# Kernel tuning notes

Measured on AMD Instinct MI355X. Metric: run time of the kernel, lower is better.

## Reference

```python
import jax, jax.numpy as jnp
import numpy as np

ALPHA = 8.3  # depth-similarity decay from Depth-aware CNN
K = 3        # kernel size
PAD = 1      # padding (stride=1, dilation=1)


def _patches(x, k, pad):
    """Extract kxk stride-1 patches. x: (B,C,H,W) -> (B,C,k,k,H,W)."""
    B, C, H, W = x.shape
    xp = jnp.pad(x, ((0, 0), (0, 0), (pad, pad), (pad, pad)))
    rows = []
    for i in range(k):
        cols = [xp[:, :, i:i + H, j:j + W] for j in range(k)]
        rows.append(jnp.stack(cols, axis=2))          # (B,C,k,H,W)
    return jnp.stack(rows, axis=2)                     # (B,C,k,k,H,W)


def setup_inputs() -> dict:
    key = jax.random.key(0)
    k1, k2, k3 = jax.random.split(key, 3)
    B, Cin, H, W = 8, 512, 64, 64
    Cout = 64
    x = jax.random.normal(k1, (B, Cin, H, W), dtype=jnp.float32)
    depth = jax.random.uniform(k2, (B, 1, H, W), dtype=jnp.float32)
    stdv = 1.0 / np.sqrt(Cin * K * K)
    weight = jax.random.uniform(k3, (Cout, Cin, K, K), dtype=jnp.float32,
                                minval=-stdv, maxval=stdv)
    return {"input": x, "depth": depth, "weight": weight}


def reference(input, depth, weight):
    # depth-modulated conv: out(p0) = sum_pn w(pn) * x(p0+pn) * exp(-a*|d(p0)-d(p0+pn)|)
    xpat = _patches(input, K, PAD)                 # (B,Cin,K,K,H,W)
    dpat = _patches(depth, K, PAD)                 # (B,1,K,K,H,W)
    d0 = depth[:, :, None, None, :, :]             # center depth (B,1,1,1,H,W)
    gate = jnp.exp(-ALPHA * jnp.abs(d0 - dpat))    # (B,1,K,K,H,W)
    out = jnp.einsum('ocij,bcijhw->bohw', weight, xpat * gate)
    return out
```

## Files before the change

### kernel.cpp

```cpp
#include <hip/hip_runtime.h>
#include <math.h>

#define ALPHA 8.3f
#define STAGE_BYTES 26112

typedef short v8s  __attribute__((ext_vector_type(8)));
typedef float v16f __attribute__((ext_vector_type(16)));
typedef float v4f  __attribute__((ext_vector_type(4)));

static __device__ __forceinline__ unsigned short f2bf(float f) {
    unsigned int u = __float_as_uint(f);
    u = (u + 0x7fffu + ((u >> 16) & 1u)) >> 16;
    return (unsigned short)u;
}

static __device__ __forceinline__ void async16(const void* g, void* l) {
    __builtin_amdgcn_global_load_lds(
        (const __attribute__((address_space(1))) unsigned int*)g,
        (__attribute__((address_space(3))) unsigned int*)l, 16, 0, 0);
}

__global__ void prep_weights(const float* __restrict__ w, unsigned short* __restrict__ wt) {
    int i = blockIdx.x * 256 + threadIdx.x;
    if (i >= 9 * 32 * 2 * 64 * 8) return;
    int j    = i & 7;
    int lane = (i >> 3) & 63;
    int mt   = (i >> 9) & 1;
    int ks   = (i >> 10) & 31;
    int tap  = i >> 15;
    int o = mt * 32 + (lane & 31);
    int c = ks * 16 + (lane >> 5) * 8 + j;
    wt[i] = f2bf(w[(o * 512 + c) * 9 + tap]);
}

__global__ __launch_bounds__(256) void nhwc_cast(const float* __restrict__ x,
                                                 unsigned short* __restrict__ x2) {
    __shared__ float st[64][65];
    const int h = blockIdx.x & 63;
    const int b = blockIdx.x >> 6;
    const int tid = threadIdx.x;
    const float* xb = x + ((size_t)b * 512) * 4096 + h * 64;
    unsigned short* ob = x2 + (((size_t)b * 64 + h) * 64) * 512;
    for (int cb = 0; cb < 8; ++cb) {
        __syncthreads();
#pragma unroll
        for (int i = 0; i < 16; ++i) {
            const int c = i * 4 + (tid >> 6);
            st[c][tid & 63] = xb[(size_t)(cb * 64 + c) * 4096 + (tid & 63)];
        }
        __syncthreads();
#pragma unroll
        for (int j = 0; j < 2; ++j) {
            const int idx = j * 256 + tid;
            const int w = idx >> 3, k = idx & 7;
            unsigned short t[8];
#pragma unroll
            for (int e = 0; e < 8; ++e) t[e] = f2bf(st[k * 8 + e][w]);
            uint4 u;
            u.x = t[0] | ((unsigned)t[1] << 16);
            u.y = t[2] | ((unsigned)t[3] << 16);
            u.z = t[4] | ((unsigned)t[5] << 16);
            u.w = t[6] | ((unsigned)t[7] << 16);
            *(uint4*)&ob[(size_t)w * 512 + cb * 64 + k * 8] = u;
        }
    }
}

__global__ __launch_bounds__(512, 2)
void depthconv_v5(const unsigned short* __restrict__ x2,
                  const float* __restrict__ depth,
                  const unsigned short* __restrict__ wt,
                  const float* __restrict__ zbuf,
                  float* __restrict__ out) {
    __shared__ __align__(16) char smem[2 * STAGE_BYTES];

    const int bx   = blockIdx.x;
    const int xcd  = bx & 7;
    const int i0   = bx >> 3;
    const int wt2  = i0 & 1;
    const int b    = (i0 >> 1) & 7;
    const int ht   = xcd * 2 + (i0 >> 4);
    const int h0 = ht * 4, w0 = wt2 * 32;

    const int tid  = threadIdx.x;
    const int wid  = tid >> 6;
    const int lane = tid & 63;
    const int l31  = lane & 31;
    const int half = lane >> 5;
    const int mt   = wid & 1;
    const int rt   = (wid >> 1) & 1;
    const int kh   = wid >> 2;

    const char* xpix = (const char*)(x2 + ((size_t)b * 4096) * 512);

    float gt[2][9];
    {
        const float* dp = depth + (size_t)b * 4096;
#pragma unroll
        for (int nt = 0; nt < 2; ++nt) {
            const int hq = h0 + 2 * rt + nt, wq = w0 + l31;
            const float d0 = dp[hq * 64 + wq];
#pragma unroll
            for (int t = 0; t < 9; ++t) {
                const int hn = hq + t / 3 - 1, wn = wq + t % 3 - 1;
                const float dn = (hn >= 0 && hn < 64 && wn >= 0 && wn < 64) ? dp[hn * 64 + wn] : 0.f;
                gt[nt][t] = __expf(-ALPHA * fabsf(d0 - dn));
            }
        }
    }

    v16f acc[2];
    v16f vzero;
#pragma unroll
    for (int r = 0; r < 16; ++r) { acc[0][r] = 0.f; acc[1][r] = 0.f; vzero[r] = 0.f; }

#define ISSUE(SS)                                                               \
    {                                                                           \
        const int ss_ = (SS);                                                   \
        char* bufb = smem + (ss_ & 1) * STAGE_BYTES;                            \
        _Pragma("unroll")                                                       \
        for (int it = 0; it < 4; ++it) {                                        \
            const int i = it * 512 + tid;                                       \
            if (i < 1632) {                                                     \
                const int slice = i >> 3;                                       \
                const int gg = (i & 7) ^ (slice & 7);                           \
                const int r = slice / 34;                                       \
                const int c = slice - r * 34;                                   \
                const int hh = h0 - 1 + r, ww = w0 - 1 + c;                     \
                const char* gp = (hh >= 0 && hh < 64 && ww >= 0 && ww < 64)     \
                    ? xpix + (size_t)(hh * 64 + ww) * 1024                      \
                           + (gg >> 2) * 512 + ss_ * 64 + (gg & 3) * 16        \
                    : (const char*)zbuf;                                        \
                async16(gp, bufb + it * 8192 + wid * 1024 + lane * 16);         \
            }                                                                   \
        }                                                                       \
    }

    ISSUE(0);

    for (int ss = 0; ss < 8; ++ss) {
        __syncthreads();
        if (ss < 7) ISSUE(ss + 1);
        const char* bufb = smem + (ss & 1) * STAGE_BYTES;
        const int ks0 = kh * 16 + ss * 2;
#pragma unroll
        for (int tap = 0; tap < 9; ++tap) {
            const int di = tap / 3, dj = tap % 3;
            const v8s a0 = *(const v8s*)&wt[(((tap * 32 + ks0) * 2 + mt) * 64 + lane) * 8];
            const v8s a1 = *(const v8s*)&wt[(((tap * 32 + ks0 + 1) * 2 + mt) * 64 + lane) * 8];
#pragma unroll
            for (int nt = 0; nt < 2; ++nt) {
                const int slice = (2 * rt + nt + di) * 34 + l31 + dj;
                const int s7 = slice & 7;
                const int g0 = kh * 4 + half;
                const int g1 = g0 + 2;
                const v8s b0 = *(const v8s*)(bufb + ((size_t)(slice * 8 + (g0 ^ s7))) * 16);
                const v8s b1 = *(const v8s*)(bufb + ((size_t)(slice * 8 + (g1 ^ s7))) * 16);
                v16f pass = __builtin_amdgcn_mfma_f32_32x32x16_bf16(a0, b0, vzero, 0, 0, 0);
                pass = __builtin_amdgcn_mfma_f32_32x32x16_bf16(a1, b1, pass, 0, 0, 0);
                const float gv = gt[nt][tap];
#pragma unroll
                for (int r = 0; r < 16; ++r)
                    acc[nt][r] = fmaf(gv, pass[r], acc[nt][r]);
            }
        }
    }

    __syncthreads();
    float* red = (float*)smem;
    const int region = mt * 2 + rt;
    if (kh == 1) {
#pragma unroll
        for (int nt = 0; nt < 2; ++nt)
#pragma unroll
            for (int qd = 0; qd < 4; ++qd) {
                v4f v;
                v[0] = acc[nt][qd * 4];     v[1] = acc[nt][qd * 4 + 1];
                v[2] = acc[nt][qd * 4 + 2]; v[3] = acc[nt][qd * 4 + 3];
                *(v4f*)&red[(region * 2 + nt) * 1024 + lane * 16 + qd * 4] = v;
            }
    }
    __syncthreads();
    if (kh == 0) {
#pragma unroll
        for (int nt = 0; nt < 2; ++nt) {
            float* ob = out + ((size_t)b * 64) * 4096 + (h0 + 2 * rt + nt) * 64 + w0;
#pragma unroll
            for (int qd = 0; qd < 4; ++qd) {
                const v4f v = *(const v4f*)&red[(region * 2 + nt) * 1024 + lane * 16 + qd * 4];
#pragma unroll
                for (int j = 0; j < 4; ++j) {
                    const int rg = qd * 4 + j;
                    const int o = mt * 32 + (rg & 3) + 8 * (rg >> 2) + 4 * half;
                    ob[(size_t)o * 4096 + l31] = acc[nt][rg] + v[j];
                }
            }
        }
    }
}

extern "C" void kernel_launch(void* const* d_in, const int* in_sizes, int n_in,
                              void* d_out, int out_size, void* d_ws, size_t ws_size,
                              hipStream_t stream) {
    const float* x      = (const float*)d_in[0];
    const float* depth  = (const float*)d_in[1];
    const float* weight = (const float*)d_in[2];
    float* out = (float*)d_out;

    unsigned short* wtb = (unsigned short*)d_ws;
    float* zbuf         = (float*)((char*)d_ws + 786432);
    unsigned short* x2  = (unsigned short*)((char*)d_ws + (1 << 20));

    prep_weights<<<1152, 256, 0, stream>>>(weight, wtb);
    hipMemsetAsync(zbuf, 0, 1024, stream);
    nhwc_cast<<<512, 256, 0, stream>>>(x, x2);
    depthconv_v5<<<256, 512, 0, stream>>>(x2, depth, wtb, zbuf, out);
}
```

Baseline: 146.7 us.

## Double warps per conv block, split transpose across channel halves, fold memset

The main conv kernel now runs 1024 threads per block, with each wave computing one output row instead of two. This halves per-wave accumulators and gate registers and doubles the waves available to hide latency. The NHWC cast kernel is split into two blocks per row (channel halves) and uses float4 loads, and the zero-buffer memset is folded into the weight-prep kernel to drop one launch. The risk is that register limits under the new launch bounds cause spills, and that larger blocks make the barriers more costly.

Result: no change. 144.4 us (-1.6%).

```diff
diff --git a/kernel.cpp b/kernel.cpp
--- a/kernel.cpp
+++ b/kernel.cpp
@@ -20,7 +20,9 @@
         (__attribute__((address_space(3))) unsigned int*)l, 16, 0, 0);
 }
 
-__global__ void prep_weights(const float* __restrict__ w, unsigned short* __restrict__ wt) {
+__global__ void prep_weights(const float* __restrict__ w, unsigned short* __restrict__ wt,
+                             float* __restrict__ zb) {
+    if (blockIdx.x == 0) zb[threadIdx.x] = 0.f;
     int i = blockIdx.x * 256 + threadIdx.x;
     if (i >= 9 * 32 * 2 * 64 * 8) return;
     int j    = i & 7;
@@ -36,17 +38,24 @@
 __global__ __launch_bounds__(256) void nhwc_cast(const float* __restrict__ x,
                                                  unsigned short* __restrict__ x2) {
     __shared__ float st[64][65];
-    const int h = blockIdx.x & 63;
-    const int b = blockIdx.x >> 6;
+    const int bx  = blockIdx.x;
+    const int ch2 = bx & 1;
+    const int h   = (bx >> 1) & 63;
+    const int b   = bx >> 7;
     const int tid = threadIdx.x;
-    const float* xb = x + ((size_t)b * 512) * 4096 + h * 64;
-    unsigned short* ob = x2 + (((size_t)b * 64 + h) * 64) * 512;
-    for (int cb = 0; cb < 8; ++cb) {
+    const float* xb = x + ((size_t)b * 512 + ch2 * 256) * 4096 + h * 64;
+    unsigned short* ob = x2 + (((size_t)b * 64 + h) * 64) * 512 + ch2 * 256;
+    for (int cb = 0; cb < 4; ++cb) {
         __syncthreads();
 #pragma unroll
-        for (int i = 0; i < 16; ++i) {
-            const int c = i * 4 + (tid >> 6);
-            st[c][tid & 63] = xb[(size_t)(cb * 64 + c) * 4096 + (tid & 63)];
+        for (int i = 0; i < 4; ++i) {
+            const int c  = i * 16 + (tid >> 4);
+            const int w4 = (tid & 15) * 4;
+            const float4 v = *(const float4*)&xb[(size_t)(cb * 64 + c) * 4096 + w4];
+            st[c][w4]     = v.x;
+            st[c][w4 + 1] = v.y;
+            st[c][w4 + 2] = v.z;
+            st[c][w4 + 3] = v.w;
         }
         __syncthreads();
 #pragma unroll
@@ -66,8 +75,8 @@
     }
 }
 
-__global__ __launch_bounds__(512, 2)
-void depthconv_v5(const unsigned short* __restrict__ x2,
+__global__ __launch_bounds__(1024, 4)
+void depthconv_v6(const unsigned short* __restrict__ x2,
                   const float* __restrict__ depth,
                   const unsigned short* __restrict__ wt,
                   const float* __restrict__ zbuf,
@@ -88,39 +97,36 @@
     const int l31  = lane & 31;
     const int half = lane >> 5;
     const int mt   = wid & 1;
-    const int rt   = (wid >> 1) & 1;
-    const int kh   = wid >> 2;
+    const int rt   = (wid >> 1) & 3;
+    const int kh   = wid >> 3;
 
     const char* xpix = (const char*)(x2 + ((size_t)b * 4096) * 512);
 
-    float gt[2][9];
+    float gt[9];
     {
         const float* dp = depth + (size_t)b * 4096;
-#pragma unroll
-        for (int nt = 0; nt < 2; ++nt) {
-            const int hq = h0 + 2 * rt + nt, wq = w0 + l31;
-            const float d0 = dp[hq * 64 + wq];
-#pragma unroll
-            for (int t = 0; t < 9; ++t) {
-                const int hn = hq + t / 3 - 1, wn = wq + t % 3 - 1;
-                const float dn = (hn >= 0 && hn < 64 && wn >= 0 && wn < 64) ? dp[hn * 64 + wn] : 0.f;
-                gt[nt][t] = __expf(-ALPHA * fabsf(d0 - dn));
-            }
-        }
-    }
-
-    v16f acc[2];
+        const int hq = h0 + rt, wq = w0 + l31;
+        const float d0 = dp[hq * 64 + wq];
+#pragma unroll
+        for (int t = 0; t < 9; ++t) {
+            const int hn = hq + t / 3 - 1, wn = wq + t % 3 - 1;
+            const float dn = (hn >= 0 && hn < 64 && wn >= 0 && wn < 64) ? dp[hn * 64 + wn] : 0.f;
+            gt[t] = __expf(-ALPHA * fabsf(d0 - dn));
+        }
+    }
+
+    v16f acc;
     v16f vzero;
 #pragma unroll
-    for (int r = 0; r < 16; ++r) { acc[0][r] = 0.f; acc[1][r] = 0.f; vzero[r] = 0.f; }
+    for (int r = 0; r < 16; ++r) { acc[r] = 0.f; vzero[r] = 0.f; }
 
 #define ISSUE(SS)                                                               \
     {                                                                           \
         const int ss_ = (SS);                                                   \
         char* bufb = smem + (ss_ & 1) * STAGE_BYTES;                            \
         _Pragma("unroll")                                                       \
-        for (int it = 0; it < 4; ++it) {                                        \
-            const int i = it * 512 + tid;                                       \
+        for (int it = 0; it < 2; ++it) {                                        \
+            const int i = it * 1024 + tid;                                      \
             if (i < 1632) {                                                     \
                 const int slice = i >> 3;                                       \
                 const int gg = (i & 7) ^ (slice & 7);                           \
@@ -131,12 +137,15 @@
                     ? xpix + (size_t)(hh * 64 + ww) * 1024                      \
                            + (gg >> 2) * 512 + ss_ * 64 + (gg & 3) * 16        \
                     : (const char*)zbuf;                                        \
-                async16(gp, bufb + it * 8192 + wid * 1024 + lane * 16);         \
+                async16(gp, bufb + (size_t)i * 16);                             \
             }                                                                   \
         }                                                                       \
     }
 
     ISSUE(0);
+
+    const int g0 = kh * 4 + half;
+    const int g1 = g0 + 2;
 
     for (int ss = 0; ss < 8; ++ss) {
         __syncthreads();
@@ -148,52 +157,42 @@
             const int di = tap / 3, dj = tap % 3;
             const v8s a0 = *(const v8s*)&wt[(((tap * 32 + ks0) * 2 + mt) * 64 + lane) * 8];
             const v8s a1 = *(const v8s*)&wt[(((tap * 32 + ks0 + 1) * 2 + mt) * 64 + lane) * 8];
-#pragma unroll
-            for (int nt = 0; nt < 2; ++nt) {
-                const int slice = (2 * rt + nt + di) * 34 + l31 + dj;
-                const int s7 = slice & 7;
-                const int g0 = kh * 4 + half;
-                const int g1 = g0 + 2;
-                const v8s b0 = *(const v8s*)(bufb + ((size_t)(slice * 8 + (g0 ^ s7))) * 16);
-                const v8s b1 = *(const v8s*)(bufb + ((size_t)(slice * 8 + (g1 ^ s7))) * 16);
-                v16f pass = __builtin_amdgcn_mfma_f32_32x32x16_bf16(a0, b0, vzero, 0, 0, 0);
-                pass = __builtin_amdgcn_mfma_f32_32x32x16_bf16(a1, b1, pass, 0, 0, 0);
-                const float gv = gt[nt][tap];
-#pragma unroll
-                for (int r = 0; r < 16; ++r)
-                    acc[nt][r] = fmaf(gv, pass[r], acc[nt][r]);
-            }
+            const int slice = (rt + di) * 34 + l31 + dj;
+            const int s7 = slice & 7;
+            const v8s b0 = *(const v8s*)(bufb + ((size_t)(slice * 8 + (g0 ^ s7))) * 16);
+            const v8s b1 = *(const v8s*)(bufb + ((size_t)(slice * 8 + (g1 ^ s7))) * 16);
+            v16f pass = __builtin_amdgcn_mfma_f32_32x32x16_bf16(a0, b0, vzero, 0, 0, 0);
+            pass = __builtin_amdgcn_mfma_f32_32x32x16_bf16(a1, b1, pass, 0, 0, 0);
+            const float gv = gt[tap];
+#pragma unroll
+            for (int r = 0; r < 16; ++r)
+                acc[r] = fmaf(gv, pass[r], acc[r]);
         }
     }
 
     __syncthreads();
     float* red = (float*)smem;
-    const int region = mt * 2 + rt;
+    const int region = mt * 4 + rt;
     if (kh == 1) {
 #pragma unroll
-        for (int nt = 0; nt < 2; ++nt)
-#pragma unroll
-            for (int qd = 0; qd < 4; ++qd) {
-                v4f v;
-                v[0] = acc[nt][qd * 4];     v[1] = acc[nt][qd * 4 + 1];
-                v[2] = acc[nt][qd * 4 + 2]; v[3] = acc[nt][qd * 4 + 3];
-                *(v4f*)&red[(region * 2 + nt) * 1024 + lane * 16 + qd * 4] = v;
-            }
+        for (int qd = 0; qd < 4; ++qd) {
+            v4f v;
+            v[0] = acc[qd * 4];     v[1] = acc[qd * 4 + 1];
+            v[2] = acc[qd * 4 + 2]; v[3] = acc[qd * 4 + 3];
+            *(v4f*)&red[region * 1024 + lane * 16 + qd * 4] = v;
+        }
     }
     __syncthreads();
     if (kh == 0) {
-#pragma unroll
-        for (int nt = 0; nt < 2; ++nt) {
-            float* ob = out + ((size_t)b * 64) * 4096 + (h0 + 2 * rt + nt) * 64 + w0;
-#pragma unroll
-            for (int qd = 0; qd < 4; ++qd) {
-                const v4f v = *(const v4f*)&red[(region * 2 + nt) * 1024 + lane * 16 + qd * 4];
-#pragma unroll
-                for (int j = 0; j < 4; ++j) {
-                    const int rg = qd * 4 + j;
-                    const int o = mt * 32 + (rg & 3) + 8 * (rg >> 2) + 4 * half;
-                    ob[(size_t)o * 4096 + l31] = acc[nt][rg] + v[j];
-                }
+        float* ob = out + ((size_t)b * 64) * 4096 + (h0 + rt) * 64 + w0;
+#pragma unroll
+        for (int qd = 0; qd < 4; ++qd) {
+            const v4f v = *(const v4f*)&red[region * 1024 + lane * 16 + qd * 4];
+#pragma unroll
+            for (int j = 0; j < 4; ++j) {
+                const int rg = qd * 4 + j;
+                const int o = mt * 32 + (rg & 3) + 8 * (rg >> 2) + 4 * half;
+                ob[(size_t)o * 4096 + l31] = acc[rg] + v[j];
             }
         }
     }
@@ -211,8 +210,7 @@
     float* zbuf         = (float*)((char*)d_ws + 786432);
     unsigned short* x2  = (unsigned short*)((char*)d_ws + (1 << 20));
 
-    prep_weights<<<1152, 256, 0, stream>>>(weight, wtb);
-    hipMemsetAsync(zbuf, 0, 1024, stream);
-    nhwc_cast<<<512, 256, 0, stream>>>(x, x2);
-    depthconv_v5<<<256, 512, 0, stream>>>(x2, depth, wtb, zbuf, out);
-}
+    prep_weights<<<1152, 256, 0, stream>>>(weight, wtb, zbuf);
+    nhwc_cast<<<1024, 256, 0, stream>>>(x, x2);
+    depthconv_v6<<<256, 1024, 0, stream>>>(x2, depth, wtb, zbuf, out);
+}
```
